# Optimization experiments

Measured on AMD Instinct MI355X. Metric: run time of the kernel, lower is better.

Reference implementation:

```python
import jax, jax.numpy as jnp
import numpy as np

K = 9          # kernel_size (odd)
STRIDE = 1
EPS = 1e-12


def _unfold(x, k, stride, pad):
    # x: (bs, ch, H, W) -> (bs, ch, k, k, out_h, out_w); mimics F.unfold + view.
    bs, ch, H, W = x.shape
    out_h = (H + 2 * pad - k) // stride + 1
    out_w = (W + 2 * pad - k) // stride + 1
    xp = jnp.pad(x, ((0, 0), (0, 0), (pad, pad), (pad, pad)))
    rows = []
    for dy in range(k):  # fixed small loop over kernel taps
        row = [xp[:, :, dy:dy + out_h * stride:stride, dx:dx + out_w * stride:stride]
               for dx in range(k)]
        rows.append(jnp.stack(row, axis=2))
    return jnp.stack(rows, axis=2)


def setup_inputs() -> dict:
    key = jax.random.key(0)
    k1, k2 = jax.random.split(key)
    inp = jax.random.normal(k1, (2, 3, 384, 384), dtype=jnp.float32)
    sigmas = jax.random.uniform(k2, (2, 2, 384, 384), dtype=jnp.float32)
    return {"input": inp, "sigmas": sigmas}


def reference(input, sigmas):
    k, s = K, STRIDE
    pad = k // 2
    dt = input.dtype
    # inverse sigmas on strided grid
    sig_s = 1.0 / (jnp.abs(sigmas[:, 0:1, ::s, ::s]) + EPS)  # (bs,1,oh,ow)
    sig_r = 1.0 / (jnp.abs(sigmas[:, 1:2, ::s, ::s]) + EPS)
    # spatial Gaussian kernel, per-pixel sigma
    r = jnp.arange(-(k // 2), k // 2 + 1, dtype=dt)
    _1d = -0.5 * r * r
    _2d = (_1d[:, None] + _1d[None, :]).reshape(1, 1, k, k, 1, 1)
    g = jnp.exp(_2d * (sig_s * sig_s)[:, :, None, None, :, :])  # (bs,1,k,k,oh,ow)
    g = g / g.sum(axis=(2, 3), keepdims=True)
    # range (guide) Gaussian from local diff^2 summed over channels
    cols = _unfold(input, k, s, pad)                          # (bs,ch,k,k,oh,ow)
    center = cols[:, :, k // 2:k // 2 + 1, k // 2:k // 2 + 1]
    diff_sq = jnp.sum((cols - center) ** 2, axis=1, keepdims=True)
    guide = jnp.exp(-0.5 * diff_sq * (sig_r * sig_r)[:, :, None, None, :, :])
    # combine, normalize (guard empty windows), apply
    kmg = g * guide
    norm = kmg.sum(axis=(2, 3), keepdims=True)
    kmg = kmg / (norm + (norm == 0).astype(dt))
    out = jnp.sum(cols * kmg, axis=(2, 3))                    # (bs,ch,oh,ow)
    return out
```

## Files before the change

### kernel.cpp

```cpp
#include <hip/hip_runtime.h>
#include <hip/hip_bf16.h>

typedef float f32x2 __attribute__((ext_vector_type(2)));

#define IMG 384
#define KR 4
#define TW 16
#define TH 8
#define HW 24
#define HH 16
#define PRS 25
#define NE 8
#define NO 7
#define PLANE (IMG*IMG)

static __device__ __forceinline__ f32x2 mk2(float a, float b) { f32x2 r; r.x = a; r.y = b; return r; }

__global__ __launch_bounds__(192) void abf_kernel(
    const float* __restrict__ input,
    const float* __restrict__ sigmas,
    float* __restrict__ out)
{
    __shared__ f32x2 sE[3 * NE * PRS];
    __shared__ f32x2 sO[3 * NO * PRS];
    __shared__ f32x2 s_comb[2][TW * (TH/2)][4];

    const int b      = blockIdx.z;
    const int tile_x = blockIdx.x * TW;
    const int tile_y = blockIdx.y * TH;
    const int tx = threadIdx.x;
    const int ty = threadIdx.y;
    const int tz = threadIdx.z;
    const int tid = tz * 64 + ty * TW + tx;

    {
        const int sy = tid / HW;
        const int sx = tid - sy * HW;
        const int gx = tile_x + sx - KR;
        const bool okx = (gx >= 0) & (gx < IMG);
        const float* inb = input + (size_t)b * 3 * PLANE;
        float* fE = (float*)sE;
        float* fO = (float*)sO;
        #pragma unroll
        for (int c = 0; c < 3; ++c) {
            #pragma unroll
            for (int k = 0; k < 2; ++k) {
                const int hy = sy + 8 * k;
                const int gy = tile_y + hy - KR;
                float v = 0.f;
                if (okx & (gy >= 0) & (gy < IMG))
                    v = inb[c * PLANE + (gy << 8) + (gy << 7) + gx];
                fE[((c * NE + (hy >> 1)) * PRS + sx) * 2 + (hy & 1)] = v;
                if (hy >= 1 && hy <= 14)
                    fO[((c * NO + ((hy - 1) >> 1)) * PRS + sx) * 2 + ((hy - 1) & 1)] = v;
            }
        }
    }
    __syncthreads();

    const int ox  = tile_x + tx;
    const int oyA = tile_y + 2 * ty;
    const int siA = (oyA << 8) + (oyA << 7) + ox;

    const float* sgb = sigmas + (size_t)b * 2 * PLANE;
    const float ssA = sgb[siA],         ssB = sgb[siA + IMG];
    const float srA = sgb[PLANE + siA], srB = sgb[PLANE + siA + IMG];
    const float isA = __builtin_amdgcn_rcpf(fabsf(ssA) + 1e-12f);
    const float isB = __builtin_amdgcn_rcpf(fabsf(ssB) + 1e-12f);
    const float irA = __builtin_amdgcn_rcpf(fabsf(srA) + 1e-12f);
    const float irB = __builtin_amdgcn_rcpf(fabsf(srB) + 1e-12f);
    const f32x2 A = mk2(-0.72134752f * isA * isA, -0.72134752f * isB * isB);
    const f32x2 B = mk2(-0.72134752f * irA * irA, -0.72134752f * irB * irB);

    const f32x2 cen0 = sE[(0 * NE + ty + 2) * PRS + tx + 4];
    const f32x2 cen1 = sE[(1 * NE + ty + 2) * PRS + tx + 4];
    const f32x2 cen2 = sE[(2 * NE + ty + 2) * PRS + tx + 4];

    f32x2 wsum = mk2(0.f, 0.f), a0 = wsum, a1 = wsum, a2 = wsum;

    #pragma unroll 1
    for (int r = 0; r < 3; ++r) {
        const int dy = tz * 3 + r;
        const float ry = (float)(dy - KR);
        const f32x2 syA = (ry * ry) * A;

        const f32x2 *p0, *p1, *p2;
        if (dy & 1) {
            const int pr = ty + ((dy - 1) >> 1);
            p0 = &sO[(0 * NO + pr) * PRS + tx];
            p1 = &sO[(1 * NO + pr) * PRS + tx];
            p2 = &sO[(2 * NO + pr) * PRS + tx];
        } else {
            const int pr = ty + (dy >> 1);
            p0 = &sE[(0 * NE + pr) * PRS + tx];
            p1 = &sE[(1 * NE + pr) * PRS + tx];
            p2 = &sE[(2 * NE + pr) * PRS + tx];
        }

        f32x2 w0[9], w1[9], w2[9];
        #pragma unroll
        for (int j = 0; j < 9; ++j) { w0[j] = p0[j]; w1[j] = p1[j]; w2[j] = p2[j]; }

        #pragma unroll
        for (int dx = 0; dx < 9; ++dx) {
            const float rx2 = (float)((dx - KR) * (dx - KR));
            const f32x2 v0 = w0[dx], v1 = w1[dx], v2 = w2[dx];
            const f32x2 d0 = v0 - cen0;
            const f32x2 d1 = v1 - cen1;
            const f32x2 d2 = v2 - cen2;
            const f32x2 dsq = d0 * d0 + d1 * d1 + d2 * d2;
            const f32x2 arg = dsq * B + (rx2 * A + syA);
            const f32x2 w = mk2(__builtin_amdgcn_exp2f(arg.x),
                                __builtin_amdgcn_exp2f(arg.y));
            wsum += w;
            a0 += w * v0;
            a1 += w * v1;
            a2 += w * v2;
        }
    }

    const int pid = ty * TW + tx;
    if (tz > 0) {
        s_comb[tz - 1][pid][0] = wsum;
        s_comb[tz - 1][pid][1] = a0;
        s_comb[tz - 1][pid][2] = a1;
        s_comb[tz - 1][pid][3] = a2;
    }
    __syncthreads();

    if (tz == 0) {
        #pragma unroll
        for (int t = 0; t < 2; ++t) {
            wsum += s_comb[t][pid][0];
            a0   += s_comb[t][pid][1];
            a1   += s_comb[t][pid][2];
            a2   += s_comb[t][pid][3];
        }
        const f32x2 inv = mk2(__builtin_amdgcn_rcpf(wsum.x),
                              __builtin_amdgcn_rcpf(wsum.y));
        float* outb = out + (size_t)b * 3 * PLANE;
        const f32x2 o0 = a0 * inv, o1 = a1 * inv, o2 = a2 * inv;
        outb[siA]                 = o0.x;  outb[siA + IMG]             = o0.y;
        outb[PLANE + siA]         = o1.x;  outb[PLANE + siA + IMG]     = o1.y;
        outb[2 * PLANE + siA]     = o2.x;  outb[2 * PLANE + siA + IMG] = o2.y;
    }
}

extern "C" void kernel_launch(void* const* d_in, const int* in_sizes, int n_in,
                              void* d_out, int out_size, void* d_ws, size_t ws_size,
                              hipStream_t stream) {
    const float* input  = (const float*)d_in[0];
    const float* sigmas = (const float*)d_in[1];
    float* out = (float*)d_out;

    dim3 block(TW, TH / 2, 3);
    dim3 grid(IMG / TW, IMG / TH, 2);
    abf_kernel<<<grid, block, 0, stream>>>(input, sigmas, out);
}
```

Measured before the change: 15.63 us.

## Replace even/odd packed float2 layout with plain rows and sliding row reuse

The split even/odd shared-memory layout, which let each thread fetch its two vertically adjacent pixels as one float2, is replaced by a single padded float array. Each thread now loads rows into registers and reuses each loaded row for both of its output pixels across consecutive taps, loading 4 rows instead of 6 row pairs. The packed f32x2 arithmetic becomes explicit scalar FMAs. This cuts LDS traffic but gives up packed-math instructions and may change register pressure.

```diff
diff --git a/kernel.cpp b/kernel.cpp
--- a/kernel.cpp
+++ b/kernel.cpp
@@ -1,7 +1,5 @@
 #include <hip/hip_runtime.h>
 #include <hip/hip_bf16.h>
-
-typedef float f32x2 __attribute__((ext_vector_type(2)));
 
 #define IMG 384
 #define KR 4
@@ -9,21 +7,16 @@
 #define TH 8
 #define HW 24
 #define HH 16
-#define PRS 25
-#define NE 8
-#define NO 7
+#define PST 37
 #define PLANE (IMG*IMG)
-
-static __device__ __forceinline__ f32x2 mk2(float a, float b) { f32x2 r; r.x = a; r.y = b; return r; }
 
 __global__ __launch_bounds__(192) void abf_kernel(
     const float* __restrict__ input,
     const float* __restrict__ sigmas,
     float* __restrict__ out)
 {
-    __shared__ f32x2 sE[3 * NE * PRS];
-    __shared__ f32x2 sO[3 * NO * PRS];
-    __shared__ f32x2 s_comb[2][TW * (TH/2)][4];
+    __shared__ float s_in[3 * HH * PST];
+    __shared__ float s_comb[2][64][9];
 
     const int b      = blockIdx.z;
     const int tile_x = blockIdx.x * TW;
@@ -39,110 +32,103 @@
         const int gx = tile_x + sx - KR;
         const bool okx = (gx >= 0) & (gx < IMG);
         const float* inb = input + (size_t)b * 3 * PLANE;
-        float* fE = (float*)sE;
-        float* fO = (float*)sO;
         #pragma unroll
         for (int c = 0; c < 3; ++c) {
             #pragma unroll
             for (int k = 0; k < 2; ++k) {
-                const int hy = sy + 8 * k;
-                const int gy = tile_y + hy - KR;
+                const int y  = sy + 8 * k;
+                const int gy = tile_y + y - KR;
                 float v = 0.f;
                 if (okx & (gy >= 0) & (gy < IMG))
                     v = inb[c * PLANE + (gy << 8) + (gy << 7) + gx];
-                fE[((c * NE + (hy >> 1)) * PRS + sx) * 2 + (hy & 1)] = v;
-                if (hy >= 1 && hy <= 14)
-                    fO[((c * NO + ((hy - 1) >> 1)) * PRS + sx) * 2 + ((hy - 1) & 1)] = v;
+                s_in[(c * HH + y) * PST + sx] = v;
             }
         }
     }
     __syncthreads();
 
     const int ox  = tile_x + tx;
-    const int oyA = tile_y + 2 * ty;
-    const int siA = (oyA << 8) + (oyA << 7) + ox;
+    const int YA  = tile_y + 2 * ty;
+    const int siA = (YA << 8) + (YA << 7) + ox;
 
     const float* sgb = sigmas + (size_t)b * 2 * PLANE;
-    const float ssA = sgb[siA],         ssB = sgb[siA + IMG];
-    const float srA = sgb[PLANE + siA], srB = sgb[PLANE + siA + IMG];
-    const float isA = __builtin_amdgcn_rcpf(fabsf(ssA) + 1e-12f);
-    const float isB = __builtin_amdgcn_rcpf(fabsf(ssB) + 1e-12f);
-    const float irA = __builtin_amdgcn_rcpf(fabsf(srA) + 1e-12f);
-    const float irB = __builtin_amdgcn_rcpf(fabsf(srB) + 1e-12f);
-    const f32x2 A = mk2(-0.72134752f * isA * isA, -0.72134752f * isB * isB);
-    const f32x2 B = mk2(-0.72134752f * irA * irA, -0.72134752f * irB * irB);
+    const float isa = __builtin_amdgcn_rcpf(fabsf(sgb[siA])         + 1e-12f);
+    const float isb = __builtin_amdgcn_rcpf(fabsf(sgb[siA + IMG])   + 1e-12f);
+    const float ira = __builtin_amdgcn_rcpf(fabsf(sgb[PLANE + siA]) + 1e-12f);
+    const float irb = __builtin_amdgcn_rcpf(fabsf(sgb[PLANE + siA + IMG]) + 1e-12f);
+    const float Aa = -0.72134752f * isa * isa, Ab = -0.72134752f * isb * isb;
+    const float Ba = -0.72134752f * ira * ira, Bb = -0.72134752f * irb * irb;
 
-    const f32x2 cen0 = sE[(0 * NE + ty + 2) * PRS + tx + 4];
-    const f32x2 cen1 = sE[(1 * NE + ty + 2) * PRS + tx + 4];
-    const f32x2 cen2 = sE[(2 * NE + ty + 2) * PRS + tx + 4];
+    const int ccb = (2 * ty + 4) * PST + tx + 4;
+    const float cA0 = s_in[0 * HH * PST + ccb],       cB0 = s_in[0 * HH * PST + ccb + PST];
+    const float cA1 = s_in[1 * HH * PST + ccb],       cB1 = s_in[1 * HH * PST + ccb + PST];
+    const float cA2 = s_in[2 * HH * PST + ccb],       cB2 = s_in[2 * HH * PST + ccb + PST];
 
-    f32x2 wsum = mk2(0.f, 0.f), a0 = wsum, a1 = wsum, a2 = wsum;
+    float wsA = 0.f, aA0 = 0.f, aA1 = 0.f, aA2 = 0.f;
+    float wsB = 0.f, aB0 = 0.f, aB1 = 0.f, aB2 = 0.f;
 
-    #pragma unroll 1
-    for (int r = 0; r < 3; ++r) {
-        const int dy = tz * 3 + r;
-        const float ry = (float)(dy - KR);
-        const f32x2 syA = (ry * ry) * A;
+    auto loadrow = [&](float (&dst)[3][9], int hy) {
+        const int base = hy * PST + tx;
+        #pragma unroll
+        for (int c = 0; c < 3; ++c)
+            #pragma unroll
+            for (int j = 0; j < 9; ++j)
+                dst[c][j] = s_in[c * HH * PST + base + j];
+    };
 
-        const f32x2 *p0, *p1, *p2;
-        if (dy & 1) {
-            const int pr = ty + ((dy - 1) >> 1);
-            p0 = &sO[(0 * NO + pr) * PRS + tx];
-            p1 = &sO[(1 * NO + pr) * PRS + tx];
-            p2 = &sO[(2 * NO + pr) * PRS + tx];
-        } else {
-            const int pr = ty + (dy >> 1);
-            p0 = &sE[(0 * NE + pr) * PRS + tx];
-            p1 = &sE[(1 * NE + pr) * PRS + tx];
-            p2 = &sE[(2 * NE + pr) * PRS + tx];
-        }
-
-        f32x2 w0[9], w1[9], w2[9];
-        #pragma unroll
-        for (int j = 0; j < 9; ++j) { w0[j] = p0[j]; w1[j] = p1[j]; w2[j] = p2[j]; }
-
+    auto dotaps = [&](const float (&ra)[3][9], const float (&rb)[3][9], int dy) {
+        const float ry  = (float)(dy - KR);
+        const float sya = ry * ry * Aa;
+        const float syb = ry * ry * Ab;
         #pragma unroll
         for (int dx = 0; dx < 9; ++dx) {
             const float rx2 = (float)((dx - KR) * (dx - KR));
-            const f32x2 v0 = w0[dx], v1 = w1[dx], v2 = w2[dx];
-            const f32x2 d0 = v0 - cen0;
-            const f32x2 d1 = v1 - cen1;
-            const f32x2 d2 = v2 - cen2;
-            const f32x2 dsq = d0 * d0 + d1 * d1 + d2 * d2;
-            const f32x2 arg = dsq * B + (rx2 * A + syA);
-            const f32x2 w = mk2(__builtin_amdgcn_exp2f(arg.x),
-                                __builtin_amdgcn_exp2f(arg.y));
-            wsum += w;
-            a0 += w * v0;
-            a1 += w * v1;
-            a2 += w * v2;
+            const float va0 = ra[0][dx], va1 = ra[1][dx], va2 = ra[2][dx];
+            const float da0 = va0 - cA0, da1 = va1 - cA1, da2 = va2 - cA2;
+            const float dsa = fmaf(da0, da0, fmaf(da1, da1, da2 * da2));
+            const float wa  = __builtin_amdgcn_exp2f(fmaf(dsa, Ba, fmaf(rx2, Aa, sya)));
+            wsA += wa; aA0 = fmaf(wa, va0, aA0); aA1 = fmaf(wa, va1, aA1); aA2 = fmaf(wa, va2, aA2);
+            const float vb0 = rb[0][dx], vb1 = rb[1][dx], vb2 = rb[2][dx];
+            const float db0 = vb0 - cB0, db1 = vb1 - cB1, db2 = vb2 - cB2;
+            const float dsb = fmaf(db0, db0, fmaf(db1, db1, db2 * db2));
+            const float wb  = __builtin_amdgcn_exp2f(fmaf(dsb, Bb, fmaf(rx2, Ab, syb)));
+            wsB += wb; aB0 = fmaf(wb, vb0, aB0); aB1 = fmaf(wb, vb1, aB1); aB2 = fmaf(wb, vb2, aB2);
         }
+    };
+
+    {
+        const int R = 2 * ty + 3 * tz;
+        float rA[3][9], rB[3][9];
+        loadrow(rA, R);
+        loadrow(rB, R + 1);
+        dotaps(rA, rB, 3 * tz);
+        loadrow(rA, R + 2);
+        dotaps(rB, rA, 3 * tz + 1);
+        loadrow(rB, R + 3);
+        dotaps(rA, rB, 3 * tz + 2);
     }
 
     const int pid = ty * TW + tx;
     if (tz > 0) {
-        s_comb[tz - 1][pid][0] = wsum;
-        s_comb[tz - 1][pid][1] = a0;
-        s_comb[tz - 1][pid][2] = a1;
-        s_comb[tz - 1][pid][3] = a2;
+        float* d = s_comb[tz - 1][pid];
+        d[0] = wsA; d[1] = aA0; d[2] = aA1; d[3] = aA2;
+        d[4] = wsB; d[5] = aB0; d[6] = aB1; d[7] = aB2;
     }
     __syncthreads();
 
     if (tz == 0) {
         #pragma unroll
         for (int t = 0; t < 2; ++t) {
-            wsum += s_comb[t][pid][0];
-            a0   += s_comb[t][pid][1];
-            a1   += s_comb[t][pid][2];
-            a2   += s_comb[t][pid][3];
+            const float* s = s_comb[t][pid];
+            wsA += s[0]; aA0 += s[1]; aA1 += s[2]; aA2 += s[3];
+            wsB += s[4]; aB0 += s[5]; aB1 += s[6]; aB2 += s[7];
         }
-        const f32x2 inv = mk2(__builtin_amdgcn_rcpf(wsum.x),
-                              __builtin_amdgcn_rcpf(wsum.y));
+        const float ivA = __builtin_amdgcn_rcpf(wsA);
+        const float ivB = __builtin_amdgcn_rcpf(wsB);
         float* outb = out + (size_t)b * 3 * PLANE;
-        const f32x2 o0 = a0 * inv, o1 = a1 * inv, o2 = a2 * inv;
-        outb[siA]                 = o0.x;  outb[siA + IMG]             = o0.y;
-        outb[PLANE + siA]         = o1.x;  outb[PLANE + siA + IMG]     = o1.y;
-        outb[2 * PLANE + siA]     = o2.x;  outb[2 * PLANE + siA + IMG] = o2.y;
+        outb[siA]             = aA0 * ivA;  outb[siA + IMG]             = aB0 * ivB;
+        outb[PLANE + siA]     = aA1 * ivA;  outb[PLANE + siA + IMG]     = aB1 * ivB;
+        outb[2 * PLANE + siA] = aA2 * ivA;  outb[2 * PLANE + siA + IMG] = aB2 * ivB;
     }
 }
 
```

Result: slower. 18.97 us (+21.4%).
